# Optimization experiments

Hardware: AMD Instinct MI355X
Metric: run time of the kernel (lower is better)

The kernel has to match this reference:

```python
import jax, jax.numpy as jnp
import numpy as np
import math

V, D, H, L, MLP = 32000, 1024, 16, 4, 4
B, T = 2, 1024
HD = D // H
ALIBI_BIAS_MAX = 8.0
EPS = 1e-5


def _ln(x, g, b):
    m = jnp.mean(x, -1, keepdims=True)
    v = jnp.mean((x - m) ** 2, -1, keepdims=True)
    return (x - m) * jax.lax.rsqrt(v + EPS) * g + b


def setup_inputs() -> dict:
    key = jax.random.key(0)
    ks = jax.random.split(key, 12)
    s = 0.02
    inp = {
        "input_ids": jax.random.randint(ks[0], (B, T), 0, V),
        "wte": jax.random.normal(ks[1], (V, D), jnp.float32) * s,
        "ln1_g": jnp.ones((L, D), jnp.float32),
        "ln1_b": jnp.zeros((L, D), jnp.float32),
        "attn_w": jax.random.normal(ks[2], (L, 3 * D, D), jnp.float32) * s,
        "attn_b": jnp.zeros((L, 3 * D), jnp.float32),
        "proj_w": jax.random.normal(ks[3], (L, D, D), jnp.float32) * s,
        "proj_b": jnp.zeros((L, D), jnp.float32),
        "ln2_g": jnp.ones((L, D), jnp.float32),
        "ln2_b": jnp.zeros((L, D), jnp.float32),
        "fc_w": jax.random.normal(ks[4], (L, MLP * D, D), jnp.float32) * s,
        "fc_b": jnp.zeros((L, MLP * D), jnp.float32),
        "fc2_w": jax.random.normal(ks[5], (L, D, MLP * D), jnp.float32) * s,
        "fc2_b": jnp.zeros((L, D), jnp.float32),
        "lnf_g": jnp.ones((D,), jnp.float32),
        "lnf_b": jnp.zeros((D,), jnp.float32),
        "lm_head_w": jax.random.normal(ks[6], (V, D), jnp.float32) * s,
    }
    return inp


def reference(input_ids, wte, ln1_g, ln1_b, attn_w, attn_b, proj_w, proj_b,
              ln2_g, ln2_b, fc_w, fc_b, fc2_w, fc2_b, lnf_g, lnf_b, lm_head_w):
    b, t = input_ids.shape
    x = wte[input_ids]  # [B,T,D]

    # causal + ALiBi bias, [H,T,T]
    pos = jnp.arange(t)
    rel = -jnp.abs(pos[None, :] - pos[:, None]).astype(jnp.float32)  # -|i-j|
    m = jnp.arange(1, H + 1, dtype=jnp.float32) * (ALIBI_BIAS_MAX / H)
    alibi = rel[None, :, :] * (2.0 ** (-m))[:, None, None]
    causal = jnp.where(pos[None, :] > pos[:, None], -jnp.inf, 0.0)
    bias = alibi + causal[None]
    scale = 1.0 / math.sqrt(HD)

    def block(x, p):
        l1g, l1b, aw, ab, pw, pb, l2g, l2b, fw, fb, f2w, f2b = p
        h = _ln(x, l1g, l1b)
        qkv = h @ aw.T + ab  # [B,T,3D]
        q, k, v = jnp.split(qkv, 3, axis=-1)
        q = q.reshape(b, t, H, HD).transpose(0, 2, 1, 3)
        k = k.reshape(b, t, H, HD).transpose(0, 2, 1, 3)
        v = v.reshape(b, t, H, HD).transpose(0, 2, 1, 3)
        att = jnp.einsum('bhid,bhjd->bhij', q, k) * scale + bias[None]
        att = jax.nn.softmax(att, axis=-1)
        y = jnp.einsum('bhij,bhjd->bhid', att, v)
        y = y.transpose(0, 2, 1, 3).reshape(b, t, D)
        x = x + (y @ pw.T + pb)
        h2 = _ln(x, l2g, l2b)
        x = x + (jax.nn.gelu(h2 @ fw.T + fb, approximate=False) @ f2w.T + f2b)
        return x, None

    x, _ = jax.lax.scan(
        block, x,
        (ln1_g, ln1_b, attn_w, attn_b, proj_w, proj_b,
         ln2_g, ln2_b, fc_w, fc_b, fc2_w, fc2_b))
    x = _ln(x, lnf_g, lnf_b)
    logits = x @ lm_head_w.T  # [B,T,V]
    return logits
```

## Files before the change

### kernel.cpp

```cpp
#include <hip/hip_runtime.h>
#include <hip/hip_bf16.h>
#include <math.h>

typedef __hip_bfloat16 bf16;
typedef __attribute__((ext_vector_type(4))) float f32x4;
typedef __attribute__((ext_vector_type(8))) short short8;

constexpr int Bc = 2, Tc = 1024, Dc = 1024, Hc = 16, Lc = 4, MLPc = 4096, Vc = 32000, HDc = 64;

__device__ __forceinline__ unsigned short f2bu(float f) {
    __hip_bfloat16 h = __float2bfloat16(f);
    unsigned short u;
    __builtin_memcpy(&u, &h, 2);
    return u;
}

__device__ __forceinline__ void gl2lds16(const bf16* g, bf16* l) {
    __builtin_amdgcn_global_load_lds(
        (const __attribute__((address_space(1))) void*)g,
        (__attribute__((address_space(3))) void*)l, 16, 0, 0);
}

enum { EPI_BIAS_BF16 = 0, EPI_GELU = 1, EPI_RESADD = 2, EPI_F32 = 3 };

template <int EPI>
__device__ __forceinline__ void epi_store(float v, int row, int col, void* Cv,
                                          int ldc, const float* bias) {
    if constexpr (EPI == EPI_BIAS_BF16) {
        v += bias[col];
        ((bf16*)Cv)[(size_t)row * ldc + col] = __float2bfloat16(v);
    } else if constexpr (EPI == EPI_GELU) {
        v += bias[col];
        v = 0.5f * v * (1.0f + erff(v * 0.70710678118f));
        ((bf16*)Cv)[(size_t)row * ldc + col] = __float2bfloat16(v);
    } else if constexpr (EPI == EPI_RESADD) {
        float* C = (float*)Cv;
        size_t idx = (size_t)row * ldc + col;
        C[idx] += v + bias[col];
    } else if constexpr (EPI == EPI_F32) {
        ((float*)Cv)[(size_t)row * ldc + col] = v;
    }
}

template <int EPI>
__global__ __launch_bounds__(512) void gemm_8p(
    const bf16* __restrict__ A, int lda,
    const bf16* __restrict__ Bm, int ldb,
    void* __restrict__ Cv, int ldc,
    const float* __restrict__ bias, int K)
{
    constexpr int BM = 256, BN = 256, BK = 64;
    __shared__ alignas(16) bf16 As[2][BM][BK];
    __shared__ alignas(16) bf16 Bs[2][BN][BK];

    const int tid = threadIdx.x;
    const int lane = tid & 63;
    const int w = tid >> 6;
    const int wm = w >> 2;
    const int wn = w & 3;

    int nwg = gridDim.x * gridDim.y;
    int orig = blockIdx.y * gridDim.x + blockIdx.x;
    int q = nwg >> 3, rr = nwg & 7, xcd = orig & 7, lid = orig >> 3;
    int wg = (xcd < rr ? xcd * (q + 1) : rr * (q + 1) + (xcd - rr) * q) + lid;
    int im = wg % gridDim.x;
    int in = wg / gridDim.x;

    const bf16* Ab = A + (size_t)im * BM * lda;
    const bf16* Bb = Bm + (size_t)in * BN * ldb;

    const int sr = lane >> 3;
    const int scs = ((lane & 7) ^ sr) * 8;
    const int lr = lane & 15, lq = lane >> 4;

    f32x4 acc[2][2][4][2];
#pragma unroll
    for (int a = 0; a < 2; a++)
#pragma unroll
        for (int b = 0; b < 2; b++)
#pragma unroll
            for (int c = 0; c < 4; c++)
#pragma unroll
                for (int d = 0; d < 2; d++) acc[a][b][c][d] = (f32x4){0.f, 0.f, 0.f, 0.f};

    const int NT = K / BK;

    auto stage_half = [&](int buf, int hf, int k0) {
        const bf16* gp = (hf & 1) ? Bb : Ab;
        const int ld = (hf & 1) ? ldb : lda;
        bf16* ls = (hf & 1) ? &Bs[buf][0][0] : &As[buf][0][0];
        const int half = hf >> 1;
#pragma unroll
        for (int i = 0; i < 2; i++) {
            int r0 = half * 128 + i * 64 + w * 8;
            gl2lds16(gp + (size_t)(r0 + sr) * ld + k0 + scs, ls + r0 * BK);
        }
    };

#pragma unroll
    for (int hf = 0; hf < 4; hf++) stage_half(0, hf, 0);
    asm volatile("s_waitcnt vmcnt(0)" ::: "memory");
    __builtin_amdgcn_s_barrier();
    asm volatile("" ::: "memory");

    for (int t = 0; t < NT; t++) {
        const int cur = t & 1;
        const char* Abase = (const char*)&As[cur][0][0];
        const char* Bbase = (const char*)&Bs[cur][0][0];
#pragma unroll
        for (int ph = 0; ph < 4; ph++) {
            const int mh = ph & 1, nh = ph >> 1;
            short8 af[4][2], bfv[2][2];
#pragma unroll
            for (int fi = 0; fi < 4; fi++) {
                int r = mh * 128 + wm * 64 + fi * 16 + lr;
#pragma unroll
                for (int kk = 0; kk < 2; kk++) {
                    int cb = (kk * 64 + lq * 16) ^ ((r & 7) << 4);
                    af[fi][kk] = *reinterpret_cast<const short8*>(Abase + (size_t)r * 128 + cb);
                }
            }
#pragma unroll
            for (int fj = 0; fj < 2; fj++) {
                int r = nh * 128 + wn * 32 + fj * 16 + lr;
#pragma unroll
                for (int kk = 0; kk < 2; kk++) {
                    int cb = (kk * 64 + lq * 16) ^ ((r & 7) << 4);
                    bfv[fj][kk] = *reinterpret_cast<const short8*>(Bbase + (size_t)r * 128 + cb);
                }
            }
            if (t + 1 < NT) stage_half(cur ^ 1, ph, (t + 1) * BK);
            __builtin_amdgcn_s_barrier();
            __builtin_amdgcn_s_setprio(1);
#pragma unroll
            for (int kk = 0; kk < 2; kk++)
#pragma unroll
                for (int fi = 0; fi < 4; fi++)
#pragma unroll
                    for (int fj = 0; fj < 2; fj++)
                        acc[mh][nh][fi][fj] = __builtin_amdgcn_mfma_f32_16x16x32_bf16(
                            af[fi][kk], bfv[fj][kk], acc[mh][nh][fi][fj], 0, 0, 0);
            __builtin_amdgcn_s_setprio(0);
            if (ph != 2) asm volatile("s_waitcnt vmcnt(4)" ::: "memory");
            __builtin_amdgcn_s_barrier();
            asm volatile("" ::: "memory");
        }
    }

#pragma unroll
    for (int mh = 0; mh < 2; mh++)
#pragma unroll
        for (int nh = 0; nh < 2; nh++)
#pragma unroll
            for (int fi = 0; fi < 4; fi++)
#pragma unroll
                for (int fj = 0; fj < 2; fj++)
#pragma unroll
                    for (int r = 0; r < 4; r++) {
                        int row = im * 256 + mh * 128 + wm * 64 + fi * 16 + lq * 4 + r;
                        int col = in * 256 + nh * 128 + wn * 32 + fj * 16 + lr;
                        epi_store<EPI>(acc[mh][nh][fi][fj][r], row, col, Cv, ldc, bias);
                    }
}

template <int BM, int BN, int BK, int EPI, bool SWZG>
__global__ __launch_bounds__(256) void gemm_fast(
    const bf16* __restrict__ A, int lda,
    const bf16* __restrict__ Bm, int ldb,
    void* __restrict__ Cv, int ldc,
    const float* __restrict__ bias, int K)
{
    static_assert(BK == 64, "staging geometry assumes BK=64");
    __shared__ alignas(16) bf16 As[2][BM][BK];
    __shared__ alignas(16) bf16 Bs[2][BN][BK];

    const int tid = threadIdx.x;
    const int lane = tid & 63;
    const int w = tid >> 6;
    const int wm = w >> 1, wn = w & 1;
    constexpr int WM = BM / 2, WN = BN / 2;
    constexpr int FM = WM / 16, FN = WN / 16;
    constexpr int RPI = 512 / BK;
    constexpr int AI = BM / (4 * RPI);
    constexpr int BI = BN / (4 * RPI);

    int im, in;
    if constexpr (SWZG) {
        int nwg = gridDim.x * gridDim.y;
        int orig = blockIdx.y * gridDim.x + blockIdx.x;
        int q = nwg >> 3, rr = nwg & 7, xcd = orig & 7, lid = orig >> 3;
        int wg = (xcd < rr ? xcd * (q + 1) : rr * (q + 1) + (xcd - rr) * q) + lid;
        im = wg % gridDim.x;
        in = wg / gridDim.x;
    } else {
        im = blockIdx.y;
        in = blockIdx.x;
    }

    const bf16* Ab = A + (size_t)im * BM * lda;
    const bf16* Bb = Bm + (size_t)in * BN * ldb;

    const int sr = lane >> 3;
    const int scs = (((lane & 7) ^ sr) * 8);
    const int lr = lane & 15, lq = lane >> 4;

    f32x4 acc[FM][FN];
#pragma unroll
    for (int i = 0; i < FM; i++)
#pragma unroll
        for (int j = 0; j < FN; j++) acc[i][j] = (f32x4){0.f, 0.f, 0.f, 0.f};

    auto stage = [&](int buf, int k0) {
#pragma unroll
        for (int i = 0; i < AI; i++) {
            int row = (w * AI + i) * RPI;
            gl2lds16(Ab + (size_t)(row + sr) * lda + k0 + scs, &As[buf][row][0]);
        }
#pragma unroll
        for (int i = 0; i < BI; i++) {
            int row = (w * BI + i) * RPI;
            gl2lds16(Bb + (size_t)(row + sr) * ldb + k0 + scs, &Bs[buf][row][0]);
        }
    };

    const int NT = K / BK;
    stage(0, 0);
    __syncthreads();

    for (int t = 0; t < NT; t++) {
        const int cur = t & 1;
        if (t + 1 < NT) stage(cur ^ 1, (t + 1) * BK);

        const char* Abase = (const char*)&As[cur][0][0];
        const char* Bbase = (const char*)&Bs[cur][0][0];
#pragma unroll
        for (int kk = 0; kk < BK / 32; kk++) {
            short8 af[FM], bfr[FN];
#pragma unroll
            for (int i = 0; i < FM; i++) {
                int r = wm * WM + i * 16 + lr;
                int cb = (kk * 64 + lq * 16) ^ ((r & 7) << 4);
                af[i] = *reinterpret_cast<const short8*>(Abase + (size_t)r * (BK * 2) + cb);
            }
#pragma unroll
            for (int j = 0; j < FN; j++) {
                int r = wn * WN + j * 16 + lr;
                int cb = (kk * 64 + lq * 16) ^ ((r & 7) << 4);
                bfr[j] = *reinterpret_cast<const short8*>(Bbase + (size_t)r * (BK * 2) + cb);
            }
#pragma unroll
            for (int i = 0; i < FM; i++)
#pragma unroll
                for (int j = 0; j < FN; j++)
                    acc[i][j] = __builtin_amdgcn_mfma_f32_16x16x32_bf16(af[i], bfr[j], acc[i][j], 0, 0, 0);
        }
        __syncthreads();
    }

#pragma unroll
    for (int i = 0; i < FM; i++)
#pragma unroll
        for (int j = 0; j < FN; j++)
#pragma unroll
            for (int r = 0; r < 4; r++) {
                int row = im * BM + wm * WM + i * 16 + lq * 4 + r;
                int col = in * BN + wn * WN + j * 16 + lr;
                epi_store<EPI>(acc[i][j][r], row, col, Cv, ldc, bias);
            }
}

template <int BM, int BN, int BK, int EPI>
__global__ __launch_bounds__(256) void gemm_bt_f32(
    const bf16* __restrict__ A, int lda,
    const float* __restrict__ Bm, int ldb,
    void* __restrict__ Cv, int ldc,
    const float* __restrict__ bias, int K)
{
    constexpr int BKP = BK + 8;
    __shared__ bf16 As[BM][BKP];
    __shared__ bf16 Bs[BN][BKP];
    const int tid = threadIdx.x;
    const int lane = tid & 63;
    const int w = tid >> 6;
    const int wm = w >> 1, wn = w & 1;
    constexpr int WM = BM / 2, WN = BN / 2;
    constexpr int FM = WM / 16, FN = WN / 16;
    const int bx = blockIdx.x, by = blockIdx.y;
    const bf16* Ab = A + (size_t)by * BM * lda;
    const float* Bb = Bm + (size_t)bx * BN * ldb;
    f32x4 acc[FM][FN];
#pragma unroll
    for (int i = 0; i < FM; i++)
#pragma unroll
        for (int j = 0; j < FN; j++) acc[i][j] = (f32x4){0.f, 0.f, 0.f, 0.f};
    const int lr = lane & 15, lq = lane >> 4;
    for (int k0 = 0; k0 < K; k0 += BK) {
        constexpr int AC = (BM * BK) / (256 * 8);
#pragma unroll
        for (int i = 0; i < AC; i++) {
            int c = tid + i * 256;
            int row = c / (BK / 8);
            int kc = (c % (BK / 8)) * 8;
            *reinterpret_cast<int4*>(&As[row][kc]) =
                *reinterpret_cast<const int4*>(Ab + (size_t)row * lda + k0 + kc);
        }
        constexpr int BC = (BN * BK) / (256 * 4);
#pragma unroll
        for (int i = 0; i < BC; i++) {
            int c = tid + i * 256;
            int row = c / (BK / 4);
            int kc = (c % (BK / 4)) * 4;
            float4 v = *reinterpret_cast<const float4*>(Bb + (size_t)row * ldb + k0 + kc);
            unsigned long long p = (unsigned long long)f2bu(v.x) |
                                   ((unsigned long long)f2bu(v.y) << 16) |
                                   ((unsigned long long)f2bu(v.z) << 32) |
                                   ((unsigned long long)f2bu(v.w) << 48);
            *reinterpret_cast<unsigned long long*>(&Bs[row][kc]) = p;
        }
        __syncthreads();
#pragma unroll
        for (int kk = 0; kk < BK / 32; kk++) {
            short8 af[FM], bfr[FN];
#pragma unroll
            for (int i = 0; i < FM; i++)
                af[i] = *reinterpret_cast<const short8*>(&As[wm * WM + i * 16 + lr][kk * 32 + lq * 8]);
#pragma unroll
            for (int j = 0; j < FN; j++)
                bfr[j] = *reinterpret_cast<const short8*>(&Bs[wn * WN + j * 16 + lr][kk * 32 + lq * 8]);
#pragma unroll
            for (int i = 0; i < FM; i++)
#pragma unroll
                for (int j = 0; j < FN; j++)
                    acc[i][j] = __builtin_amdgcn_mfma_f32_16x16x32_bf16(af[i], bfr[j], acc[i][j], 0, 0, 0);
        }
        __syncthreads();
    }
#pragma unroll
    for (int i = 0; i < FM; i++)
#pragma unroll
        for (int j = 0; j < FN; j++)
#pragma unroll
            for (int r = 0; r < 4; r++) {
                int row = by * BM + wm * WM + i * 16 + lq * 4 + r;
                int col = bx * BN + wn * WN + j * 16 + lr;
                epi_store<EPI>(acc[i][j][r], row, col, Cv, ldc, bias);
            }
}

__global__ __launch_bounds__(256) void flash_attn(
    const bf16* __restrict__ q, const bf16* __restrict__ kbuf,
    const bf16* __restrict__ vt, bf16* __restrict__ y)
{
    __shared__ alignas(16) bf16 Ks[128 * 64];
    __shared__ alignas(16) bf16 Vs[64 * 128];
    __shared__ alignas(16) bf16 Ps[4 * 16 * 136];

    const int tid = threadIdx.x;
    const int lane = tid & 63;
    const int w = tid >> 6;
    const int lr = lane & 15, lq = lane >> 4;
    const int qi = (int)gridDim.x - 1 - (int)blockIdx.x;
    const int z = blockIdx.y;
    const int b = z >> 4, h = z & 15;
    const float slope = exp2f(-0.5f * (float)(h + 1));

    const bf16* qz = q + (size_t)z * (Tc * HDc);
    const bf16* kz = kbuf + (size_t)z * (Tc * HDc);
    const bf16* vz = vt + (size_t)z * (HDc * Tc);

    const int rowbase = qi * 64 + w * 16;

    short8 qf[2];
#pragma unroll
    for (int kk = 0; kk < 2; kk++)
        qf[kk] = *reinterpret_cast<const short8*>(
            qz + (size_t)(rowbase + lr) * HDc + kk * 32 + lq * 8);

    float m_old[4], l_sum[4];
#pragma unroll
    for (int r = 0; r < 4; r++) { m_old[r] = -3.0e38f; l_sum[r] = 0.f; }
    f32x4 o[4];
#pragma unroll
    for (int dj = 0; dj < 4; dj++) o[dj] = (f32x4){0.f, 0.f, 0.f, 0.f};

    bf16* Pw = Ps + w * 16 * 136;

    const int nkv = (qi * 64 + 63) / 128 + 1;
    for (int kv = 0; kv < nkv; kv++) {
#pragma unroll
        for (int i = 0; i < 4; i++) {
            int rbase = w * 32 + i * 8;
            int row = rbase + (lane >> 3);
            int slot = lane & 7;
            gl2lds16(kz + (size_t)(kv * 128 + row) * HDc + ((slot ^ (row & 7)) * 8),
                     &Ks[rbase * 64]);
        }
#pragma unroll
        for (int i = 0; i < 4; i++) {
            int rbase = w * 16 + i * 4;
            int row = rbase + lq;
            gl2lds16(vz + (size_t)row * Tc + kv * 128 + ((lr ^ (row & 7)) * 8),
                     &Vs[rbase * 128]);
        }
        __syncthreads();

        f32x4 s[8];
#pragma unroll
        for (int j = 0; j < 8; j++) s[j] = (f32x4){0.f, 0.f, 0.f, 0.f};
#pragma unroll
        for (int kk = 0; kk < 2; kk++) {
#pragma unroll
            for (int j = 0; j < 8; j++) {
                int row = j * 16 + lr;
                int cb = ((kk * 4 + lq) ^ (row & 7)) << 4;
                short8 bfr = *reinterpret_cast<const short8*>(
                    (const char*)Ks + row * 128 + cb);
                s[j] = __builtin_amdgcn_mfma_f32_16x16x32_bf16(qf[kk], bfr, s[j], 0, 0, 0);
            }
        }

        float mt[4];
#pragma unroll
        for (int r = 0; r < 4; r++) mt[r] = -3.0e38f;
#pragma unroll
        for (int j = 0; j < 8; j++) {
            int col = kv * 128 + j * 16 + lr;
#pragma unroll
            for (int r = 0; r < 4; r++) {
                int rowg = rowbase + lq * 4 + r;
                float v = s[j][r] * 0.125f - (float)(rowg - col) * slope;
                v = (col > rowg) ? -3.0e38f : v;
                s[j][r] = v;
                mt[r] = fmaxf(mt[r], v);
            }
        }
#pragma unroll
        for (int r = 0; r < 4; r++)
#pragma unroll
            for (int off = 1; off < 16; off <<= 1)
                mt[r] = fmaxf(mt[r], __shfl_xor(mt[r], off));

        float f[4], rs[4];
#pragma unroll
        for (int r = 0; r < 4; r++) {
            float mn = fmaxf(m_old[r], mt[r]);
            f[r] = __expf(m_old[r] - mn);
            m_old[r] = mn;
            rs[r] = 0.f;
        }
#pragma unroll
        for (int j = 0; j < 8; j++)
#pragma unroll
            for (int r = 0; r < 4; r++) {
                float p = __expf(s[j][r] - m_old[r]);
                s[j][r] = p;
                rs[r] += p;
            }
#pragma unroll
        for (int r = 0; r < 4; r++) {
#pragma unroll
            for (int off = 1; off < 16; off <<= 1)
                rs[r] += __shfl_xor(rs[r], off);
            l_sum[r] = l_sum[r] * f[r] + rs[r];
        }

#pragma unroll
        for (int j = 0; j < 8; j++)
#pragma unroll
            for (int r = 0; r < 4; r++)
                Pw[(lq * 4 + r) * 136 + j * 16 + lr] = __float2bfloat16(s[j][r]);

#pragma unroll
        for (int dj = 0; dj < 4; dj++)
#pragma unroll
            for (int r = 0; r < 4; r++) o[dj][r] *= f[r];

        __syncthreads();

#pragma unroll
        for (int kk = 0; kk < 4; kk++) {
            short8 pa = *reinterpret_cast<const short8*>(
                (const char*)Pw + lr * 272 + kk * 64 + lq * 16);
#pragma unroll
            for (int dj = 0; dj < 4; dj++) {
                int row = dj * 16 + lr;
                int cb = ((kk * 4 + lq) ^ (row & 7)) << 4;
                short8 vb = *reinterpret_cast<const short8*>(
                    (const char*)Vs + row * 256 + cb);
                o[dj] = __builtin_amdgcn_mfma_f32_16x16x32_bf16(pa, vb, o[dj], 0, 0, 0);
            }
        }
        __syncthreads();
    }

#pragma unroll
    for (int dj = 0; dj < 4; dj++)
#pragma unroll
        for (int r = 0; r < 4; r++) {
            int rowg = rowbase + lq * 4 + r;
            float outv = o[dj][r] / l_sum[r];
            y[((size_t)b * Tc + rowg) * Dc + h * HDc + dj * 16 + lr] =
                __float2bfloat16(outv);
        }
}

__global__ __launch_bounds__(256) void f2b8(const float* __restrict__ in,
                                            bf16* __restrict__ out, long n) {
    long i = ((long)blockIdx.x * 256 + threadIdx.x) * 8;
    if (i >= n) return;
    float4 a = *reinterpret_cast<const float4*>(in + i);
    float4 b = *reinterpret_cast<const float4*>(in + i + 4);
    unsigned long long p0 = (unsigned long long)f2bu(a.x) |
                            ((unsigned long long)f2bu(a.y) << 16) |
                            ((unsigned long long)f2bu(a.z) << 32) |
                            ((unsigned long long)f2bu(a.w) << 48);
    unsigned long long p1 = (unsigned long long)f2bu(b.x) |
                            ((unsigned long long)f2bu(b.y) << 16) |
                            ((unsigned long long)f2bu(b.z) << 32) |
                            ((unsigned long long)f2bu(b.w) << 48);
    *reinterpret_cast<unsigned long long*>(out + i) = p0;
    *reinterpret_cast<unsigned long long*>(out + i + 4) = p1;
}

__global__ __launch_bounds__(256) void embed_kernel(const int* __restrict__ ids,
                                                    const float* __restrict__ wte,
                                                    float* __restrict__ x) {
    int row = blockIdx.x;
    int t = threadIdx.x;
    int id = ids[row];
    reinterpret_cast<float4*>(x + (size_t)row * Dc)[t] =
        reinterpret_cast<const float4*>(wte + (size_t)id * Dc)[t];
}

__global__ __launch_bounds__(256) void ln_kernel(const float* __restrict__ x,
                                                 const float* __restrict__ g,
                                                 const float* __restrict__ b,
                                                 bf16* __restrict__ out) {
    int row = blockIdx.x;
    int t = threadIdx.x;
    const float4 v = reinterpret_cast<const float4*>(x + (size_t)row * Dc)[t];
    float s = v.x + v.y + v.z + v.w;
    float s2 = v.x * v.x + v.y * v.y + v.z * v.z + v.w * v.w;
#pragma unroll
    for (int o = 32; o > 0; o >>= 1) {
        s += __shfl_down(s, o);
        s2 += __shfl_down(s2, o);
    }
    __shared__ float sm[8];
    int wid = t >> 6, ln = t & 63;
    if (ln == 0) { sm[wid] = s; sm[4 + wid] = s2; }
    __syncthreads();
    if (t == 0) {
        float ts = sm[0] + sm[1] + sm[2] + sm[3];
        float ts2 = sm[4] + sm[5] + sm[6] + sm[7];
        sm[0] = ts; sm[4] = ts2;
    }
    __syncthreads();
    float mean = sm[0] * (1.0f / Dc);
    float var = sm[4] * (1.0f / Dc) - mean * mean;
    float rstd = rsqrtf(var + 1e-5f);
    int c0 = t * 4;
    float vv[4] = {v.x, v.y, v.z, v.w};
    unsigned long long p = 0;
#pragma unroll
    for (int j = 0; j < 4; j++) {
        float val = (vv[j] - mean) * rstd * g[c0 + j] + b[c0 + j];
        p |= (unsigned long long)f2bu(val) << (16 * j);
    }
    *reinterpret_cast<unsigned long long*>(out + (size_t)row * Dc + c0) = p;
}

__global__ __launch_bounds__(256) void unpack_qkv(const bf16* __restrict__ qkv,
                                                  bf16* __restrict__ q,
                                                  bf16* __restrict__ k,
                                                  bf16* __restrict__ vt) {
    int idx = blockIdx.x * 256 + threadIdx.x;
    {
        int bt = idx >> 7;
        int c = idx & 127;
        int b = bt >> 10, t = bt & (Tc - 1);
        int h = c >> 3;
        int hd = (c & 7) * 8;
        size_t dst = (((size_t)(b * Hc + h) * Tc + t) * HDc + hd) / 8;
        const int4* src = reinterpret_cast<const int4*>(qkv + (size_t)bt * 3 * Dc);
        reinterpret_cast<int4*>(q)[dst] = src[c];
        reinterpret_cast<int4*>(k)[dst] = src[128 + c];
    }
    {
        int t0 = (idx & 127) * 8;
        int rest = idx >> 7;
        int hd = rest & 63;
        int z = rest >> 6;
        int b = z >> 4, h = z & 15;
        const bf16* src = qkv + ((size_t)b * Tc) * 3 * Dc + 2 * Dc + h * HDc + hd;
        unsigned long long p0 = 0, p1 = 0;
#pragma unroll
        for (int i = 0; i < 4; i++) {
            unsigned short u;
            __builtin_memcpy(&u, src + (size_t)(t0 + i) * 3 * Dc, 2);
            p0 |= (unsigned long long)u << (16 * i);
        }
#pragma unroll
        for (int i = 0; i < 4; i++) {
            unsigned short u;
            __builtin_memcpy(&u, src + (size_t)(t0 + 4 + i) * 3 * Dc, 2);
            p1 |= (unsigned long long)u << (16 * i);
        }
        bf16* dst = vt + ((size_t)z * HDc + hd) * Tc + t0;
        *reinterpret_cast<unsigned long long*>(dst) = p0;
        *reinterpret_cast<unsigned long long*>(dst + 4) = p1;
    }
}

extern "C" void kernel_launch(void* const* d_in, const int* in_sizes, int n_in,
                              void* d_out, int out_size, void* d_ws, size_t ws_size,
                              hipStream_t stream) {
    const int* ids = (const int*)d_in[0];
    const float* wte = (const float*)d_in[1];
    const float* ln1g = (const float*)d_in[2];
    const float* ln1b = (const float*)d_in[3];
    const float* attw = (const float*)d_in[4];
    const float* attb = (const float*)d_in[5];
    const float* projw = (const float*)d_in[6];
    const float* projb = (const float*)d_in[7];
    const float* ln2g = (const float*)d_in[8];
    const float* ln2b = (const float*)d_in[9];
    const float* fcw = (const float*)d_in[10];
    const float* fcb = (const float*)d_in[11];
    const float* fc2w = (const float*)d_in[12];
    const float* fc2b = (const float*)d_in[13];
    const float* lnfg = (const float*)d_in[14];
    const float* lnfb = (const float*)d_in[15];
    const float* lmw = (const float*)d_in[16];

    const int M = Bc * Tc;
    char* ws = (char*)d_ws;
    size_t off = 0;
    auto carve = [&](size_t bytes) { char* p = ws + off; off += (bytes + 255) & ~(size_t)255; return p; };

    float* x = (float*)carve((size_t)M * Dc * 4);
    bf16* h = (bf16*)carve((size_t)M * Dc * 2);
    bf16* qkv = (bf16*)carve((size_t)M * 3 * Dc * 2);
    bf16* q = (bf16*)carve((size_t)Bc * Hc * Tc * HDc * 2);
    bf16* kb = (bf16*)carve((size_t)Bc * Hc * Tc * HDc * 2);
    bf16* vt = (bf16*)carve((size_t)Bc * Hc * Tc * HDc * 2);
    bf16* y = (bf16*)carve((size_t)M * Dc * 2);
    bf16* mlp = (bf16*)carve((size_t)M * MLPc * 2);

    const long nLM = (long)Vc * Dc;
    bool has_wlm = ws_size >= off + (size_t)nLM * 2;
    bf16* wlm = nullptr;
    if (has_wlm) wlm = (bf16*)carve((size_t)nLM * 2);

    const long nAW = (long)Lc * 3 * Dc * Dc;
    const long nPW = (long)Lc * Dc * Dc;
    const long nFW = (long)Lc * MLPc * Dc;
    const long nF2W = (long)Lc * Dc * MLPc;
    bf16* awAll = (bf16*)d_out;
    bf16* pwAll = awAll + nAW;
    bf16* fwAll = pwAll + nPW;
    bf16* f2wAll = fwAll + nFW;

    embed_kernel<<<M, 256, 0, stream>>>(ids, wte, x);

    f2b8<<<(int)(nAW / 8 / 256), 256, 0, stream>>>(attw, awAll, nAW);
    f2b8<<<(int)(nPW / 8 / 256), 256, 0, stream>>>(projw, pwAll, nPW);
    f2b8<<<(int)(nFW / 8 / 256), 256, 0, stream>>>(fcw, fwAll, nFW);
    f2b8<<<(int)(nF2W / 8 / 256), 256, 0, stream>>>(fc2w, f2wAll, nF2W);
    if (has_wlm)
        f2b8<<<(int)(nLM / 8 / 256), 256, 0, stream>>>(lmw, wlm, nLM);

    for (int l = 0; l < Lc; l++) {
        bf16* aw_b = awAll + (size_t)l * 3 * Dc * Dc;
        bf16* pw_b = pwAll + (size_t)l * Dc * Dc;
        bf16* fw_b = fwAll + (size_t)l * MLPc * Dc;
        bf16* f2w_b = f2wAll + (size_t)l * Dc * MLPc;

        ln_kernel<<<M, 256, 0, stream>>>(x, ln1g + l * Dc, ln1b + l * Dc, h);

        gemm_fast<128, 128, 64, EPI_BIAS_BF16, true>
            <<<dim3(M / 128, 3 * Dc / 128, 1), 256, 0, stream>>>(
                h, Dc, aw_b, Dc, qkv, 3 * Dc, attb + l * 3 * Dc, Dc);

        unpack_qkv<<<(M * Dc / 8) / 256, 256, 0, stream>>>(qkv, q, kb, vt);

        flash_attn<<<dim3(Tc / 64, Bc * Hc), 256, 0, stream>>>(q, kb, vt, y);

        gemm_fast<128, 128, 64, EPI_RESADD, true>
            <<<dim3(M / 128, Dc / 128, 1), 256, 0, stream>>>(
                y, Dc, pw_b, Dc, x, Dc, projb + l * Dc, Dc);

        ln_kernel<<<M, 256, 0, stream>>>(x, ln2g + l * Dc, ln2b + l * Dc, h);

        gemm_fast<128, 128, 64, EPI_GELU, true>
            <<<dim3(M / 128, MLPc / 128, 1), 256, 0, stream>>>(
                h, Dc, fw_b, Dc, mlp, MLPc, fcb + l * MLPc, Dc);

        gemm_fast<128, 128, 64, EPI_RESADD, true>
            <<<dim3(M / 128, Dc / 128, 1), 256, 0, stream>>>(
                mlp, MLPc, f2w_b, MLPc, x, Dc, fc2b + l * Dc, MLPc);
    }

    ln_kernel<<<M, 256, 0, stream>>>(x, lnfg, lnfb, h);

    if (has_wlm)
        gemm_8p<EPI_F32>
            <<<dim3(M / 256, Vc / 256, 1), 512, 0, stream>>>(
                h, Dc, wlm, Dc, (float*)d_out, Vc, nullptr, Dc);
    else
        gemm_bt_f32<128, 128, 64, EPI_F32>
            <<<dim3(Vc / 128, M / 128, 1), 256, 0, stream>>>(
                h, Dc, lmw, Dc, (float*)d_out, Vc, nullptr, Dc);
}
```

Measured before the change: 1.298 ms.

## Fuse QKV unpack into GEMM epilogue and reuse MFMA fragments across phases

The QKV projection GEMM now writes its bias-added bf16 outputs straight into head-major Q and K buffers and a transposed V buffer, so the separate unpack_qkv kernel and the intermediate qkv buffer are gone. This removes one launch per layer and a full write-then-read of the QKV activations. The cost is scattered per-element stores in the epilogue, and the V transpose writes are strided. The 256x256 gemm_8p main loop is also reordered into a snake pattern (00, 01, 11, 10) so A or B fragments loaded from LDS are reused across consecutive phases, cutting LDS reads per k-tile.

```diff
diff --git a/kernel.cpp b/kernel.cpp
--- a/kernel.cpp
+++ b/kernel.cpp
@@ -21,7 +21,7 @@
         (__attribute__((address_space(3))) void*)l, 16, 0, 0);
 }
 
-enum { EPI_BIAS_BF16 = 0, EPI_GELU = 1, EPI_RESADD = 2, EPI_F32 = 3 };
+enum { EPI_BIAS_BF16 = 0, EPI_GELU = 1, EPI_RESADD = 2, EPI_F32 = 3, EPI_QKV = 4 };
 
 template <int EPI>
 __device__ __forceinline__ void epi_store(float v, int row, int col, void* Cv,
@@ -39,7 +39,60 @@
         C[idx] += v + bias[col];
     } else if constexpr (EPI == EPI_F32) {
         ((float*)Cv)[(size_t)row * ldc + col] = v;
-    }
+    } else if constexpr (EPI == EPI_QKV) {
+        v += bias[col];
+        bf16 bv = __float2bfloat16(v);
+        int b = row >> 10, t = row & 1023;
+        int seg = col >> 10;
+        int cc = col & 1023;
+        int h = cc >> 6, hd = cc & 63;
+        bf16* base = (bf16*)Cv;
+        if (seg == 0)
+            base[((size_t)(b * Hc + h) * Tc + t) * HDc + hd] = bv;
+        else if (seg == 1)
+            base[2097152 + ((size_t)(b * Hc + h) * Tc + t) * HDc + hd] = bv;
+        else
+            base[4194304 + ((size_t)(b * Hc + h) * HDc + hd) * Tc + t] = bv;
+    }
+}
+
+template <int MH>
+__device__ __forceinline__ void load_af8(short8 (&af)[4][2], const char* Abase,
+                                         int wm, int lr, int lq) {
+#pragma unroll
+    for (int fi = 0; fi < 4; fi++) {
+        int r = MH * 128 + wm * 64 + fi * 16 + lr;
+#pragma unroll
+        for (int kk = 0; kk < 2; kk++) {
+            int cb = (kk * 64 + lq * 16) ^ ((r & 7) << 4);
+            af[fi][kk] = *reinterpret_cast<const short8*>(Abase + (size_t)r * 128 + cb);
+        }
+    }
+}
+template <int NH>
+__device__ __forceinline__ void load_bf4(short8 (&bfv)[2][2], const char* Bbase,
+                                         int wn, int lr, int lq) {
+#pragma unroll
+    for (int fj = 0; fj < 2; fj++) {
+        int r = NH * 128 + wn * 32 + fj * 16 + lr;
+#pragma unroll
+        for (int kk = 0; kk < 2; kk++) {
+            int cb = (kk * 64 + lq * 16) ^ ((r & 7) << 4);
+            bfv[fj][kk] = *reinterpret_cast<const short8*>(Bbase + (size_t)r * 128 + cb);
+        }
+    }
+}
+template <int MH, int NH>
+__device__ __forceinline__ void mma16(f32x4 (&acc)[2][2][4][2],
+                                      const short8 (&af)[4][2], const short8 (&bfv)[2][2]) {
+#pragma unroll
+    for (int kk = 0; kk < 2; kk++)
+#pragma unroll
+        for (int fi = 0; fi < 4; fi++)
+#pragma unroll
+            for (int fj = 0; fj < 2; fj++)
+                acc[MH][NH][fi][fj] = __builtin_amdgcn_mfma_f32_16x16x32_bf16(
+                    af[fi][kk], bfv[fj][kk], acc[MH][NH][fi][fj], 0, 0, 0);
 }
 
 template <int EPI>
@@ -85,11 +138,12 @@
 
     const int NT = K / BK;
 
-    auto stage_half = [&](int buf, int hf, int k0) {
-        const bf16* gp = (hf & 1) ? Bb : Ab;
-        const int ld = (hf & 1) ? ldb : lda;
-        bf16* ls = (hf & 1) ? &Bs[buf][0][0] : &As[buf][0][0];
-        const int half = hf >> 1;
+    auto stage_half = [&](int buf, int sg, int k0) {
+        const bool isB = (sg == 1 || sg == 2);
+        const bf16* gp = isB ? Bb : Ab;
+        const int ld = isB ? ldb : lda;
+        bf16* ls = isB ? &Bs[buf][0][0] : &As[buf][0][0];
+        const int half = (sg == 2 || sg == 3) ? 1 : 0;
 #pragma unroll
         for (int i = 0; i < 2; i++) {
             int r0 = half * 128 + i * 64 + w * 8;
@@ -98,53 +152,56 @@
     };
 
 #pragma unroll
-    for (int hf = 0; hf < 4; hf++) stage_half(0, hf, 0);
+    for (int sg = 0; sg < 4; sg++) stage_half(0, sg, 0);
     asm volatile("s_waitcnt vmcnt(0)" ::: "memory");
     __builtin_amdgcn_s_barrier();
     asm volatile("" ::: "memory");
+
+    short8 af[4][2], bfv[2][2];
 
     for (int t = 0; t < NT; t++) {
         const int cur = t & 1;
         const char* Abase = (const char*)&As[cur][0][0];
         const char* Bbase = (const char*)&Bs[cur][0][0];
-#pragma unroll
-        for (int ph = 0; ph < 4; ph++) {
-            const int mh = ph & 1, nh = ph >> 1;
-            short8 af[4][2], bfv[2][2];
-#pragma unroll
-            for (int fi = 0; fi < 4; fi++) {
-                int r = mh * 128 + wm * 64 + fi * 16 + lr;
-#pragma unroll
-                for (int kk = 0; kk < 2; kk++) {
-                    int cb = (kk * 64 + lq * 16) ^ ((r & 7) << 4);
-                    af[fi][kk] = *reinterpret_cast<const short8*>(Abase + (size_t)r * 128 + cb);
-                }
-            }
-#pragma unroll
-            for (int fj = 0; fj < 2; fj++) {
-                int r = nh * 128 + wn * 32 + fj * 16 + lr;
-#pragma unroll
-                for (int kk = 0; kk < 2; kk++) {
-                    int cb = (kk * 64 + lq * 16) ^ ((r & 7) << 4);
-                    bfv[fj][kk] = *reinterpret_cast<const short8*>(Bbase + (size_t)r * 128 + cb);
-                }
-            }
-            if (t + 1 < NT) stage_half(cur ^ 1, ph, (t + 1) * BK);
-            __builtin_amdgcn_s_barrier();
-            __builtin_amdgcn_s_setprio(1);
-#pragma unroll
-            for (int kk = 0; kk < 2; kk++)
-#pragma unroll
-                for (int fi = 0; fi < 4; fi++)
-#pragma unroll
-                    for (int fj = 0; fj < 2; fj++)
-                        acc[mh][nh][fi][fj] = __builtin_amdgcn_mfma_f32_16x16x32_bf16(
-                            af[fi][kk], bfv[fj][kk], acc[mh][nh][fi][fj], 0, 0, 0);
-            __builtin_amdgcn_s_setprio(0);
-            if (ph != 2) asm volatile("s_waitcnt vmcnt(4)" ::: "memory");
-            __builtin_amdgcn_s_barrier();
-            asm volatile("" ::: "memory");
-        }
+        const bool pf = (t + 1 < NT);
+        const int kn = (t + 1) * BK;
+
+        load_af8<0>(af, Abase, wm, lr, lq);
+        load_bf4<0>(bfv, Bbase, wn, lr, lq);
+        if (pf) stage_half(cur ^ 1, 0, kn);
+        __builtin_amdgcn_s_barrier();
+        __builtin_amdgcn_s_setprio(1);
+        mma16<0, 0>(acc, af, bfv);
+        __builtin_amdgcn_s_setprio(0);
+        asm volatile("s_waitcnt vmcnt(4)" ::: "memory");
+        __builtin_amdgcn_s_barrier();
+
+        load_bf4<1>(bfv, Bbase, wn, lr, lq);
+        if (pf) stage_half(cur ^ 1, 1, kn);
+        __builtin_amdgcn_s_barrier();
+        __builtin_amdgcn_s_setprio(1);
+        mma16<0, 1>(acc, af, bfv);
+        __builtin_amdgcn_s_setprio(0);
+        asm volatile("s_waitcnt vmcnt(4)" ::: "memory");
+        __builtin_amdgcn_s_barrier();
+
+        load_af8<1>(af, Abase, wm, lr, lq);
+        if (pf) stage_half(cur ^ 1, 2, kn);
+        __builtin_amdgcn_s_barrier();
+        __builtin_amdgcn_s_setprio(1);
+        mma16<1, 1>(acc, af, bfv);
+        __builtin_amdgcn_s_setprio(0);
+        asm volatile("" ::: "memory");
+        __builtin_amdgcn_s_barrier();
+
+        load_bf4<0>(bfv, Bbase, wn, lr, lq);
+        if (pf) stage_half(cur ^ 1, 3, kn);
+        __builtin_amdgcn_s_barrier();
+        __builtin_amdgcn_s_setprio(1);
+        mma16<1, 0>(acc, af, bfv);
+        __builtin_amdgcn_s_setprio(0);
+        asm volatile("s_waitcnt vmcnt(4)" ::: "memory");
+        __builtin_amdgcn_s_barrier();
     }
 
 #pragma unroll
@@ -570,48 +627,6 @@
     *reinterpret_cast<unsigned long long*>(out + (size_t)row * Dc + c0) = p;
 }
 
-__global__ __launch_bounds__(256) void unpack_qkv(const bf16* __restrict__ qkv,
-                                                  bf16* __restrict__ q,
-                                                  bf16* __restrict__ k,
-                                                  bf16* __restrict__ vt) {
-    int idx = blockIdx.x * 256 + threadIdx.x;
-    {
-        int bt = idx >> 7;
-        int c = idx & 127;
-        int b = bt >> 10, t = bt & (Tc - 1);
-        int h = c >> 3;
-        int hd = (c & 7) * 8;
-        size_t dst = (((size_t)(b * Hc + h) * Tc + t) * HDc + hd) / 8;
-        const int4* src = reinterpret_cast<const int4*>(qkv + (size_t)bt * 3 * Dc);
-        reinterpret_cast<int4*>(q)[dst] = src[c];
-        reinterpret_cast<int4*>(k)[dst] = src[128 + c];
-    }
-    {
-        int t0 = (idx & 127) * 8;
-        int rest = idx >> 7;
-        int hd = rest & 63;
-        int z = rest >> 6;
-        int b = z >> 4, h = z & 15;
-        const bf16* src = qkv + ((size_t)b * Tc) * 3 * Dc + 2 * Dc + h * HDc + hd;
-        unsigned long long p0 = 0, p1 = 0;
-#pragma unroll
-        for (int i = 0; i < 4; i++) {
-            unsigned short u;
-            __builtin_memcpy(&u, src + (size_t)(t0 + i) * 3 * Dc, 2);
-            p0 |= (unsigned long long)u << (16 * i);
-        }
-#pragma unroll
-        for (int i = 0; i < 4; i++) {
-            unsigned short u;
-            __builtin_memcpy(&u, src + (size_t)(t0 + 4 + i) * 3 * Dc, 2);
-            p1 |= (unsigned long long)u << (16 * i);
-        }
-        bf16* dst = vt + ((size_t)z * HDc + hd) * Tc + t0;
-        *reinterpret_cast<unsigned long long*>(dst) = p0;
-        *reinterpret_cast<unsigned long long*>(dst + 4) = p1;
-    }
-}
-
 extern "C" void kernel_launch(void* const* d_in, const int* in_sizes, int n_in,
                               void* d_out, int out_size, void* d_ws, size_t ws_size,
                               hipStream_t stream) {
@@ -640,12 +655,12 @@
 
     float* x = (float*)carve((size_t)M * Dc * 4);
     bf16* h = (bf16*)carve((size_t)M * Dc * 2);
-    bf16* qkv = (bf16*)carve((size_t)M * 3 * Dc * 2);
     bf16* q = (bf16*)carve((size_t)Bc * Hc * Tc * HDc * 2);
     bf16* kb = (bf16*)carve((size_t)Bc * Hc * Tc * HDc * 2);
     bf16* vt = (bf16*)carve((size_t)Bc * Hc * Tc * HDc * 2);
     bf16* y = (bf16*)carve((size_t)M * Dc * 2);
     bf16* mlp = (bf16*)carve((size_t)M * MLPc * 2);
+    (void)kb; (void)vt;
 
     const long nLM = (long)Vc * Dc;
     bool has_wlm = ws_size >= off + (size_t)nLM * 2;
@@ -678,11 +693,9 @@
 
         ln_kernel<<<M, 256, 0, stream>>>(x, ln1g + l * Dc, ln1b + l * Dc, h);
 
-        gemm_fast<128, 128, 64, EPI_BIAS_BF16, true>
+        gemm_fast<128, 128, 64, EPI_QKV, true>
             <<<dim3(M / 128, 3 * Dc / 128, 1), 256, 0, stream>>>(
-                h, Dc, aw_b, Dc, qkv, 3 * Dc, attb + l * 3 * Dc, Dc);
-
-        unpack_qkv<<<(M * Dc / 8) / 256, 256, 0, stream>>>(qkv, q, kb, vt);
+                h, Dc, aw_b, Dc, q, 0, attb + l * 3 * Dc, Dc);
 
         flash_attn<<<dim3(Tc / 64, Bc * Hc), 256, 0, stream>>>(q, kb, vt, y);
 
```

New measurement: 1.282 ms. No clear change (-1.2%).
